# Kernel tuning notes

Measured on AMD Instinct MI355X. Metric: run time of the kernel, lower is better.

The kernel has to match this reference:

```python
import jax, jax.numpy as jnp
import numpy as np

N_NODES = 50000
N_EDGES = 800000
IN_CH = 16
OUT_CH = 16


def setup_inputs() -> dict:
    key = jax.random.key(0)
    ks = jax.random.split(key, 12)
    s = lambda d: 1.0 / np.sqrt(d)
    return {
        "x": jax.random.normal(ks[0], (N_NODES, IN_CH), jnp.float32),
        "edge_index": jax.random.randint(ks[1], (2, N_EDGES), 0, N_NODES, jnp.int64),
        "edge_attr": jax.random.uniform(ks[2], (N_EDGES, 8), jnp.float32),
        "W1": jax.random.normal(ks[3], (8, 100), jnp.float32) * s(8),
        "b1": jnp.zeros((100,), jnp.float32),
        "W2": jax.random.normal(ks[4], (100, 100), jnp.float32) * s(100),
        "b2": jnp.zeros((100,), jnp.float32),
        "W3": jax.random.normal(ks[5], (100, 100), jnp.float32) * s(100),
        "b3": jnp.zeros((100,), jnp.float32),
        "W4": jax.random.normal(ks[6], (100, IN_CH * OUT_CH), jnp.float32) * s(100),
        "b4": jnp.zeros((IN_CH * OUT_CH,), jnp.float32),
        "root": jax.random.normal(ks[7], (IN_CH, OUT_CH), jnp.float32) * s(IN_CH),
        "bias": jnp.zeros((OUT_CH,), jnp.float32),
    }


def reference(x, edge_index, edge_attr, W1, b1, W2, b2, W3, b3, W4, b4, root, bias):
    src, dst = edge_index[0], edge_index[1]
    # edge MLP -> per-edge weight matrix [E, in, out]
    h = jax.nn.relu(edge_attr @ W1 + b1)
    h = jax.nn.relu(h @ W2 + b2)
    h = jax.nn.relu(h @ W3 + b3)
    w = (h @ W4 + b4).reshape(-1, IN_CH, OUT_CH)
    # gather source features, per-edge matmul
    msg = jnp.einsum('ei,eio->eo', x[src], w)  # [E, out]
    # scatter-mean into destination nodes
    agg = jax.ops.segment_sum(msg, dst, num_segments=N_NODES)
    cnt = jax.ops.segment_sum(jnp.ones((msg.shape[0],), msg.dtype), dst, num_segments=N_NODES)
    agg = agg / jnp.maximum(cnt, 1.0)[:, None]
    return x @ root + agg + bias
```

## Files before the change

kernel.cpp:

```cpp
#include <hip/hip_runtime.h>
#include <hip/hip_bf16.h>

constexpr int N_NODES = 50000;
constexpr int E_TOTAL = 800000;
constexpr int EB   = 128;
constexpr int NT   = E_TOTAL / EB;
constexpr int GRID = 256;
constexpr int TPB  = 512;

typedef __attribute__((ext_vector_type(8))) short bf16x8;
typedef __attribute__((ext_vector_type(4))) float f32x4;

constexpr size_t WS_CNT = 0;
constexpr size_t WS_W1  = 200704;
constexpr size_t WS_W2  = WS_W1 + 8192;
constexpr size_t WS_W3  = WS_W2 + 32768;
constexpr size_t WS_W4  = WS_W3 + 32768;

constexpr int L_W4  = 0;
constexpr int L_HA  = 69632;
constexpr int L_HB  = 104448;
constexpr int L_EA  = 139264;
constexpr int L_XS  = 149504;
constexpr int L_DST = 159744;
constexpr int L_TOT = 160768;

__device__ inline unsigned short bfb(float f) {
    __hip_bfloat16 h = __float2bfloat16(f);
    return __builtin_bit_cast(unsigned short, h);
}
__device__ inline unsigned pk2(float a, float b) {
    return (unsigned)bfb(a) | ((unsigned)bfb(b) << 16);
}

__device__ inline void stage(const char* g, char* l, int bytes, int t) {
    const int wave = t >> 6, lane = t & 63;
    for (int c = wave; c * 1024 < bytes; c += 8) {
        __builtin_amdgcn_global_load_lds(
            (const __attribute__((address_space(1))) void*)(g + c * 1024 + lane * 16),
            (__attribute__((address_space(3))) void*)(l + c * 1024), 16, 0, 0);
    }
}

template<int IN_OFF, int OUT_OFF>
__device__ inline void layerB(char* sm, const bf16x8 (&wf)[2][4],
                              int we, int wn, int lane)
{
    const int r16 = lane & 15, g4 = lane >> 4;
    f32x4 acc[2][4] = {};
#pragma unroll
    for (int ks = 0; ks < 4; ++ks) {
        bf16x8 b[4];
#pragma unroll
        for (int ef = 0; ef < 4; ++ef) {
            const int e = 64 * we + 16 * ef + r16;
            b[ef] = *reinterpret_cast<const bf16x8*>(sm + IN_OFF + e * 272 + ks * 64 + g4 * 16);
        }
#pragma unroll
        for (int mf = 0; mf < 2; ++mf)
#pragma unroll
            for (int ef = 0; ef < 4; ++ef)
                acc[mf][ef] = __builtin_amdgcn_mfma_f32_16x16x32_bf16(wf[mf][ks], b[ef], acc[mf][ef], 0, 0, 0);
    }
#pragma unroll
    for (int mf = 0; mf < 2; ++mf)
#pragma unroll
        for (int ef = 0; ef < 4; ++ef) {
            const int e = 64 * we + 16 * ef + r16;
            uint2 pk;
            pk.x = pk2(fmaxf(acc[mf][ef][0], 0.f), fmaxf(acc[mf][ef][1], 0.f));
            pk.y = pk2(fmaxf(acc[mf][ef][2], 0.f), fmaxf(acc[mf][ef][3], 0.f));
            *reinterpret_cast<uint2*>(sm + OUT_OFF + e * 272 + 64 * wn + 32 * mf + 8 * g4) = pk;
        }
}

__global__ __launch_bounds__(TPB, 2)
void edge_kernel(const float* __restrict__ x, const int* __restrict__ eidx,
                 const float* __restrict__ ea, const char* __restrict__ ws,
                 float* __restrict__ out, float* __restrict__ cnt)
{
    extern __shared__ char sm[];
    const int t    = threadIdx.x;
    const int lane = t & 63;
    const int wave = t >> 6;
    const int we   = wave >> 2, wn = wave & 3;
    const int we4  = wave >> 1, wn4 = wave & 1;
    const int r16  = lane & 15, g4 = lane >> 4;
    int* dsti = reinterpret_cast<int*>(sm + L_DST);

    bf16x8 wf1[2], wf2[2][4], wf3[2][4];
#pragma unroll
    for (int mf = 0; mf < 2; ++mf) {
        const int n = 32 * wn + 16 * mf + r16;
        wf1[mf] = *reinterpret_cast<const bf16x8*>(ws + WS_W1 + n * 64 + g4 * 16);
#pragma unroll
        for (int ks = 0; ks < 4; ++ks) {
            wf2[mf][ks] = *reinterpret_cast<const bf16x8*>(ws + WS_W2 + n * 256 + ks * 64 + g4 * 16);
            wf3[mf][ks] = *reinterpret_cast<const bf16x8*>(ws + WS_W3 + n * 256 + ks * 64 + g4 * 16);
        }
    }

    stage(ws + WS_W4, sm + L_W4, 69632, t);

    {
        const int e = t >> 2, q = t & 3;
        if (q > 0) {
            uint4 z = make_uint4(0u, 0u, 0u, 0u);
            if (q == 1) z.x = 0x3F80u;
            *reinterpret_cast<uint4*>(sm + L_EA + e * 80 + 16 * q) = z;
        }
    }

    float4 eaR, xvR; int dstR = 0;
    {
        const int e0 = blockIdx.x * EB;
        if (t < 256) eaR = *reinterpret_cast<const float4*>(&ea[(size_t)(e0 + (t >> 1)) * 8 + (t & 1) * 4]);
        const int s = eidx[e0 + (t >> 2)];
        xvR = *reinterpret_cast<const float4*>(&x[(size_t)s * 16 + (t & 3) * 4]);
        if (t < 128) dstR = eidx[E_TOTAL + e0 + t];
    }

    int p = 0;
    bool has_prev = false;
    for (int tile = blockIdx.x; tile < NT; tile += GRID) {
        if (has_prev) {
            const int e = t >> 2, o0 = (t & 3) * 4;
            const float4 s0 = *reinterpret_cast<const float4*>(sm + L_HB + e * 80 + o0 * 4);
            const float4 s1 = *reinterpret_cast<const float4*>(sm + L_HB + 10240 + e * 80 + o0 * 4);
            const int d = dsti[(p ^ 1) * 128 + e];
            unsafeAtomicAdd(&out[(size_t)d * 16 + o0 + 0], s0.x + s1.x);
            unsafeAtomicAdd(&out[(size_t)d * 16 + o0 + 1], s0.y + s1.y);
            unsafeAtomicAdd(&out[(size_t)d * 16 + o0 + 2], s0.z + s1.z);
            unsafeAtomicAdd(&out[(size_t)d * 16 + o0 + 3], s0.w + s1.w);
            if ((t & 3) == 0) unsafeAtomicAdd(&cnt[d], 1.0f);
        }
        if (t < 256) {
            uint2 pk; pk.x = pk2(eaR.x, eaR.y); pk.y = pk2(eaR.z, eaR.w);
            *reinterpret_cast<uint2*>(sm + L_EA + (t >> 1) * 80 + 8 * (t & 1)) = pk;
        }
        *reinterpret_cast<float4*>(sm + L_XS + (t >> 2) * 80 + (t & 3) * 16) = xvR;
        if (t < 128) dsti[p * 128 + t] = dstR;

        const int nxt = tile + GRID;
        if (nxt < NT) {
            const int e0 = nxt * EB;
            if (t < 256) eaR = *reinterpret_cast<const float4*>(&ea[(size_t)(e0 + (t >> 1)) * 8 + (t & 1) * 4]);
            const int s = eidx[e0 + (t >> 2)];
            xvR = *reinterpret_cast<const float4*>(&x[(size_t)s * 16 + (t & 3) * 4]);
            if (t < 128) dstR = eidx[E_TOTAL + e0 + t];
        }
        __syncthreads();

        {
            f32x4 acc[2][4] = {};
            bf16x8 b[4];
#pragma unroll
            for (int ef = 0; ef < 4; ++ef) {
                const int e = 64 * we + 16 * ef + r16;
                b[ef] = *reinterpret_cast<const bf16x8*>(sm + L_EA + e * 80 + g4 * 16);
            }
#pragma unroll
            for (int mf = 0; mf < 2; ++mf)
#pragma unroll
                for (int ef = 0; ef < 4; ++ef)
                    acc[mf][ef] = __builtin_amdgcn_mfma_f32_16x16x32_bf16(wf1[mf], b[ef], acc[mf][ef], 0, 0, 0);
#pragma unroll
            for (int mf = 0; mf < 2; ++mf)
#pragma unroll
                for (int ef = 0; ef < 4; ++ef) {
                    const int e = 64 * we + 16 * ef + r16;
                    uint2 pk;
                    pk.x = pk2(fmaxf(acc[mf][ef][0], 0.f), fmaxf(acc[mf][ef][1], 0.f));
                    pk.y = pk2(fmaxf(acc[mf][ef][2], 0.f), fmaxf(acc[mf][ef][3], 0.f));
                    *reinterpret_cast<uint2*>(sm + L_HA + e * 272 + 64 * wn + 32 * mf + 8 * g4) = pk;
                }
        }
        __syncthreads();
        layerB<L_HA, L_HB>(sm, wf2, we, wn, lane);
        __syncthreads();
        layerB<L_HB, L_HA>(sm, wf3, we, wn, lane);
        __syncthreads();

        {
            f32x4 acc[8][2] = {};
#pragma unroll
            for (int ks = 0; ks < 4; ++ks) {
                bf16x8 b[2];
#pragma unroll
                for (int ef = 0; ef < 2; ++ef) {
                    const int e = 32 * we4 + 16 * ef + r16;
                    b[ef] = *reinterpret_cast<const bf16x8*>(sm + L_HA + e * 272 + ks * 64 + g4 * 16);
                }
#pragma unroll
                for (int mf = 0; mf < 8; ++mf) {
                    const int n = 128 * wn4 + 16 * mf + r16;
                    const bf16x8 a = *reinterpret_cast<const bf16x8*>(sm + L_W4 + n * 272 + ks * 64 + g4 * 16);
#pragma unroll
                    for (int ef = 0; ef < 2; ++ef)
                        acc[mf][ef] = __builtin_amdgcn_mfma_f32_16x16x32_bf16(a, b[ef], acc[mf][ef], 0, 0, 0);
                }
            }
#pragma unroll
            for (int ef = 0; ef < 2; ++ef) {
                const int e = 32 * we4 + 16 * ef + r16;
                const float4 xa = *reinterpret_cast<const float4*>(sm + L_XS + e * 80 + 32 * wn4);
                const float4 xb = *reinterpret_cast<const float4*>(sm + L_XS + e * 80 + 32 * wn4 + 16);
                float4 mp = make_float4(0.f, 0.f, 0.f, 0.f);
#pragma unroll
                for (int mf = 0; mf < 8; ++mf) {
                    const float xi = (mf < 4) ? (&xa.x)[mf] : (&xb.x)[mf - 4];
                    mp.x = fmaf(xi, acc[mf][ef][0], mp.x);
                    mp.y = fmaf(xi, acc[mf][ef][1], mp.y);
                    mp.z = fmaf(xi, acc[mf][ef][2], mp.z);
                    mp.w = fmaf(xi, acc[mf][ef][3], mp.w);
                }
                *reinterpret_cast<float4*>(sm + L_HB + wn4 * 10240 + e * 80 + g4 * 16) = mp;
            }
        }
        __syncthreads();
        p ^= 1;
        has_prev = true;
    }

    {
        const int e = t >> 2, o0 = (t & 3) * 4;
        const float4 s0 = *reinterpret_cast<const float4*>(sm + L_HB + e * 80 + o0 * 4);
        const float4 s1 = *reinterpret_cast<const float4*>(sm + L_HB + 10240 + e * 80 + o0 * 4);
        const int d = dsti[(p ^ 1) * 128 + e];
        unsafeAtomicAdd(&out[(size_t)d * 16 + o0 + 0], s0.x + s1.x);
        unsafeAtomicAdd(&out[(size_t)d * 16 + o0 + 1], s0.y + s1.y);
        unsafeAtomicAdd(&out[(size_t)d * 16 + o0 + 2], s0.z + s1.z);
        unsafeAtomicAdd(&out[(size_t)d * 16 + o0 + 3], s0.w + s1.w);
        if ((t & 3) == 0) unsafeAtomicAdd(&cnt[d], 1.0f);
    }
}

__global__ __launch_bounds__(256)
void prep_kernel(const float* __restrict__ W1, const float* __restrict__ b1,
                 const float* __restrict__ W2, const float* __restrict__ b2,
                 const float* __restrict__ W3, const float* __restrict__ b3,
                 const float* __restrict__ W4, const float* __restrict__ b4,
                 char* __restrict__ ws)
{
    const int id = blockIdx.x * 256 + threadIdx.x;
    if (id < N_NODES) reinterpret_cast<float*>(ws + WS_CNT)[id] = 0.f;
    if (id >= 69632) return;
    if (id < 4096) {
        const int n = id >> 5, k = id & 31;
        float v = 0.f;
        if (k < 8)        { if (n < 100) v = W1[k * 100 + n]; }
        else if (k == 8)  { v = (n < 100) ? b1[n] : (n == 100 ? 1.f : 0.f); }
        reinterpret_cast<unsigned short*>(ws + WS_W1)[id] = bfb(v);
    } else if (id < 20480) {
        const int j = id - 4096, n = j >> 7, k = j & 127;
        float v = 0.f;
        if (k < 100)       { if (n < 100) v = W2[k * 100 + n]; }
        else if (k == 100) { v = (n < 100) ? b2[n] : (n == 100 ? 1.f : 0.f); }
        reinterpret_cast<unsigned short*>(ws + WS_W2)[j] = bfb(v);
    } else if (id < 36864) {
        const int j = id - 20480, n = j >> 7, k = j & 127;
        float v = 0.f;
        if (k < 100)       { if (n < 100) v = W3[k * 100 + n]; }
        else if (k == 100) { v = (n < 100) ? b3[n] : (n == 100 ? 1.f : 0.f); }
        reinterpret_cast<unsigned short*>(ws + WS_W3)[j] = bfb(v);
    } else {
        const int j = id - 36864, n = j >> 7, k = j & 127;
        float v = 0.f;
        if (k < 100)       v = W4[k * 256 + n];
        else if (k == 100) v = b4[n];
        *reinterpret_cast<unsigned short*>(ws + WS_W4 + n * 272 + 2 * k) = bfb(v);
    }
}

__global__ __launch_bounds__(256)
void node_kernel(const float* __restrict__ x, const float* __restrict__ root,
                 const float* __restrict__ bias, const float* __restrict__ cnt,
                 float* __restrict__ out)
{
    const int n = blockIdx.x * blockDim.x + threadIdx.x;
    if (n >= N_NODES) return;
    float xr[16];
#pragma unroll
    for (int q = 0; q < 4; ++q) {
        const float4 v = *reinterpret_cast<const float4*>(&x[(size_t)n * 16 + 4 * q]);
        xr[4 * q] = v.x; xr[4 * q + 1] = v.y; xr[4 * q + 2] = v.z; xr[4 * q + 3] = v.w;
    }
    const float inv = 1.f / fmaxf(cnt[n], 1.f);
#pragma unroll
    for (int q = 0; q < 4; ++q) {
        float4 o4 = *reinterpret_cast<float4*>(&out[(size_t)n * 16 + 4 * q]);
        float res[4];
#pragma unroll
        for (int j = 0; j < 4; ++j) {
            const int o = 4 * q + j;
            float dot = 0.f;
#pragma unroll
            for (int i = 0; i < 16; ++i)
                dot = fmaf(xr[i], root[i * 16 + o], dot);
            res[j] = dot + (&o4.x)[j] * inv + bias[o];
        }
        *reinterpret_cast<float4*>(&out[(size_t)n * 16 + 4 * q]) = make_float4(res[0], res[1], res[2], res[3]);
    }
}

extern "C" void kernel_launch(void* const* d_in, const int* in_sizes, int n_in,
                              void* d_out, int out_size, void* d_ws, size_t ws_size,
                              hipStream_t stream)
{
    const float* x    = (const float*)d_in[0];
    const int*   eidx = (const int*)  d_in[1];
    const float* ea   = (const float*)d_in[2];
    const float* W1   = (const float*)d_in[3];
    const float* b1   = (const float*)d_in[4];
    const float* W2   = (const float*)d_in[5];
    const float* b2   = (const float*)d_in[6];
    const float* W3   = (const float*)d_in[7];
    const float* b3   = (const float*)d_in[8];
    const float* W4   = (const float*)d_in[9];
    const float* b4   = (const float*)d_in[10];
    const float* root = (const float*)d_in[11];
    const float* bias = (const float*)d_in[12];
    float* out = (float*)d_out;
    char*  ws  = (char*)d_ws;
    float* cnt = (float*)d_ws;

    (void)in_sizes; (void)n_in; (void)ws_size;

    hipFuncSetAttribute((const void*)edge_kernel,
                        hipFuncAttributeMaxDynamicSharedMemorySize, L_TOT);

    hipMemsetAsync(d_out, 0, (size_t)out_size * sizeof(float), stream);

    hipLaunchKernelGGL(prep_kernel, dim3(272), dim3(256), 0, stream,
                       W1, b1, W2, b2, W3, b3, W4, b4, ws);
    hipLaunchKernelGGL(edge_kernel, dim3(GRID), dim3(TPB), L_TOT, stream,
                       x, eidx, ea, ws, out, cnt);
    hipLaunchKernelGGL(node_kernel, dim3((N_NODES + 255) / 256), dim3(256), 0, stream,
                       x, root, bias, cnt, out);
}
```

Measured before the change: 344.5 us.

## Switch edge MLP to 32x32x16 MFMA and keep W4 in registers

Replaces the 16x16x32 MFMA tiling with 32x32x16 tiles in all four edge-MLP layers, changing the per-wave work split, and loads the W4 fragments into registers once per wave instead of staging W4 into LDS and rereading it every tile. Removing the W4 LDS copy shrinks shared memory, and a new 4-way message buffer replaces the previous 2-way reduction before the atomics. The larger MFMA shape means fewer instructions and fewer LDS operand reads. In exchange, register pressure rises a lot: wf2, wf3 and wf4 plus the 16-float accumulators must fit under launch_bounds(512,2), so spills are possible.

```diff
diff --git a/kernel.cpp b/kernel.cpp
--- a/kernel.cpp
+++ b/kernel.cpp
@@ -8,22 +8,22 @@
 constexpr int GRID = 256;
 constexpr int TPB  = 512;
 
-typedef __attribute__((ext_vector_type(8))) short bf16x8;
-typedef __attribute__((ext_vector_type(4))) float f32x4;
+typedef __attribute__((ext_vector_type(8)))  short bf16x8;
+typedef __attribute__((ext_vector_type(16))) float f32x16;
 
 constexpr size_t WS_CNT = 0;
 constexpr size_t WS_W1  = 200704;
-constexpr size_t WS_W2  = WS_W1 + 8192;
+constexpr size_t WS_W2  = WS_W1 + 4096;
 constexpr size_t WS_W3  = WS_W2 + 32768;
 constexpr size_t WS_W4  = WS_W3 + 32768;
 
-constexpr int L_W4  = 0;
-constexpr int L_HA  = 69632;
-constexpr int L_HB  = 104448;
-constexpr int L_EA  = 139264;
-constexpr int L_XS  = 149504;
-constexpr int L_DST = 159744;
-constexpr int L_TOT = 160768;
+constexpr int L_HA  = 0;
+constexpr int L_HB  = 34816;
+constexpr int L_EA  = 69632;
+constexpr int L_XS  = 75776;
+constexpr int L_MSG = 86016;
+constexpr int L_DST = 126976;
+constexpr int L_TOT = 128000;
 
 __device__ inline unsigned short bfb(float f) {
     __hip_bfloat16 h = __float2bfloat16(f);
@@ -32,46 +32,38 @@
 __device__ inline unsigned pk2(float a, float b) {
     return (unsigned)bfb(a) | ((unsigned)bfb(b) << 16);
 }
-
-__device__ inline void stage(const char* g, char* l, int bytes, int t) {
-    const int wave = t >> 6, lane = t & 63;
-    for (int c = wave; c * 1024 < bytes; c += 8) {
-        __builtin_amdgcn_global_load_lds(
-            (const __attribute__((address_space(1))) void*)(g + c * 1024 + lane * 16),
-            (__attribute__((address_space(3))) void*)(l + c * 1024), 16, 0, 0);
-    }
+__device__ inline unsigned pk2r(float a, float b) {
+    return pk2(fmaxf(a, 0.f), fmaxf(b, 0.f));
 }
 
 template<int IN_OFF, int OUT_OFF>
-__device__ inline void layerB(char* sm, const bf16x8 (&wf)[2][4],
-                              int we, int wn, int lane)
-{
-    const int r16 = lane & 15, g4 = lane >> 4;
-    f32x4 acc[2][4] = {};
-#pragma unroll
-    for (int ks = 0; ks < 4; ++ks) {
-        bf16x8 b[4];
-#pragma unroll
-        for (int ef = 0; ef < 4; ++ef) {
-            const int e = 64 * we + 16 * ef + r16;
-            b[ef] = *reinterpret_cast<const bf16x8*>(sm + IN_OFF + e * 272 + ks * 64 + g4 * 16);
-        }
-#pragma unroll
-        for (int mf = 0; mf < 2; ++mf)
-#pragma unroll
-            for (int ef = 0; ef < 4; ++ef)
-                acc[mf][ef] = __builtin_amdgcn_mfma_f32_16x16x32_bf16(wf[mf][ks], b[ef], acc[mf][ef], 0, 0, 0);
-    }
-#pragma unroll
-    for (int mf = 0; mf < 2; ++mf)
-#pragma unroll
-        for (int ef = 0; ef < 4; ++ef) {
-            const int e = 64 * we + 16 * ef + r16;
+__device__ inline void layer32(char* sm, const bf16x8 (&wf)[8],
+                               int wn, int we, int l31, int g)
+{
+    f32x16 acc[2] = {};
+#pragma unroll
+    for (int ks = 0; ks < 8; ++ks) {
+        bf16x8 b[2];
+#pragma unroll
+        for (int ef = 0; ef < 2; ++ef) {
+            const int e = 64 * we + 32 * ef + l31;
+            b[ef] = *reinterpret_cast<const bf16x8*>(sm + IN_OFF + e * 272 + ks * 32 + g * 16);
+        }
+#pragma unroll
+        for (int ef = 0; ef < 2; ++ef)
+            acc[ef] = __builtin_amdgcn_mfma_f32_32x32x16_bf16(wf[ks], b[ef], acc[ef], 0, 0, 0);
+    }
+#pragma unroll
+    for (int ef = 0; ef < 2; ++ef) {
+        const int e = 64 * we + 32 * ef + l31;
+#pragma unroll
+        for (int q = 0; q < 4; ++q) {
             uint2 pk;
-            pk.x = pk2(fmaxf(acc[mf][ef][0], 0.f), fmaxf(acc[mf][ef][1], 0.f));
-            pk.y = pk2(fmaxf(acc[mf][ef][2], 0.f), fmaxf(acc[mf][ef][3], 0.f));
-            *reinterpret_cast<uint2*>(sm + OUT_OFF + e * 272 + 64 * wn + 32 * mf + 8 * g4) = pk;
-        }
+            pk.x = pk2r(acc[ef][4 * q + 0], acc[ef][4 * q + 1]);
+            pk.y = pk2r(acc[ef][4 * q + 2], acc[ef][4 * q + 3]);
+            *reinterpret_cast<uint2*>(sm + OUT_OFF + e * 272 + 64 * wn + 16 * q + 8 * g) = pk;
+        }
+    }
 }
 
 __global__ __launch_bounds__(TPB, 2)
@@ -83,33 +75,30 @@
     const int t    = threadIdx.x;
     const int lane = t & 63;
     const int wave = t >> 6;
-    const int we   = wave >> 2, wn = wave & 3;
-    const int we4  = wave >> 1, wn4 = wave & 1;
-    const int r16  = lane & 15, g4 = lane >> 4;
+    const int wn   = wave & 3, we = wave >> 2;
+    const int l31  = lane & 31, g = lane >> 5;
     int* dsti = reinterpret_cast<int*>(sm + L_DST);
 
-    bf16x8 wf1[2], wf2[2][4], wf3[2][4];
-#pragma unroll
-    for (int mf = 0; mf < 2; ++mf) {
-        const int n = 32 * wn + 16 * mf + r16;
-        wf1[mf] = *reinterpret_cast<const bf16x8*>(ws + WS_W1 + n * 64 + g4 * 16);
-#pragma unroll
-        for (int ks = 0; ks < 4; ++ks) {
-            wf2[mf][ks] = *reinterpret_cast<const bf16x8*>(ws + WS_W2 + n * 256 + ks * 64 + g4 * 16);
-            wf3[mf][ks] = *reinterpret_cast<const bf16x8*>(ws + WS_W3 + n * 256 + ks * 64 + g4 * 16);
-        }
-    }
-
-    stage(ws + WS_W4, sm + L_W4, 69632, t);
-
+    bf16x8 wf1, wf2[8], wf3[8], wf4[2][8];
     {
-        const int e = t >> 2, q = t & 3;
-        if (q > 0) {
-            uint4 z = make_uint4(0u, 0u, 0u, 0u);
-            if (q == 1) z.x = 0x3F80u;
-            *reinterpret_cast<uint4*>(sm + L_EA + e * 80 + 16 * q) = z;
-        }
-    }
+        const int n = 32 * wn + l31;
+        wf1 = *reinterpret_cast<const bf16x8*>(ws + WS_W1 + n * 32 + g * 16);
+#pragma unroll
+        for (int ks = 0; ks < 8; ++ks) {
+            wf2[ks] = *reinterpret_cast<const bf16x8*>(ws + WS_W2 + n * 256 + ks * 32 + g * 16);
+            wf3[ks] = *reinterpret_cast<const bf16x8*>(ws + WS_W3 + n * 256 + ks * 32 + g * 16);
+        }
+#pragma unroll
+        for (int mf = 0; mf < 2; ++mf) {
+            const int n4 = 64 * wn + 32 * mf + l31;
+#pragma unroll
+            for (int ks = 0; ks < 8; ++ks)
+                wf4[mf][ks] = *reinterpret_cast<const bf16x8*>(ws + WS_W4 + n4 * 256 + ks * 32 + g * 16);
+        }
+    }
+
+    if (t < 128)
+        *reinterpret_cast<uint4*>(sm + L_EA + t * 48 + 16) = make_uint4(0x3F80u, 0u, 0u, 0u);
 
     float4 eaR, xvR; int dstR = 0;
     {
@@ -125,18 +114,20 @@
     for (int tile = blockIdx.x; tile < NT; tile += GRID) {
         if (has_prev) {
             const int e = t >> 2, o0 = (t & 3) * 4;
-            const float4 s0 = *reinterpret_cast<const float4*>(sm + L_HB + e * 80 + o0 * 4);
-            const float4 s1 = *reinterpret_cast<const float4*>(sm + L_HB + 10240 + e * 80 + o0 * 4);
+            float4 s0 = *reinterpret_cast<const float4*>(sm + L_MSG + 0 * 10240 + e * 80 + o0 * 4);
+            const float4 s1 = *reinterpret_cast<const float4*>(sm + L_MSG + 1 * 10240 + e * 80 + o0 * 4);
+            const float4 s2 = *reinterpret_cast<const float4*>(sm + L_MSG + 2 * 10240 + e * 80 + o0 * 4);
+            const float4 s3 = *reinterpret_cast<const float4*>(sm + L_MSG + 3 * 10240 + e * 80 + o0 * 4);
             const int d = dsti[(p ^ 1) * 128 + e];
-            unsafeAtomicAdd(&out[(size_t)d * 16 + o0 + 0], s0.x + s1.x);
-            unsafeAtomicAdd(&out[(size_t)d * 16 + o0 + 1], s0.y + s1.y);
-            unsafeAtomicAdd(&out[(size_t)d * 16 + o0 + 2], s0.z + s1.z);
-            unsafeAtomicAdd(&out[(size_t)d * 16 + o0 + 3], s0.w + s1.w);
+            unsafeAtomicAdd(&out[(size_t)d * 16 + o0 + 0], s0.x + s1.x + s2.x + s3.x);
+            unsafeAtomicAdd(&out[(size_t)d * 16 + o0 + 1], s0.y + s1.y + s2.y + s3.y);
+            unsafeAtomicAdd(&out[(size_t)d * 16 + o0 + 2], s0.z + s1.z + s2.z + s3.z);
+            unsafeAtomicAdd(&out[(size_t)d * 16 + o0 + 3], s0.w + s1.w + s2.w + s3.w);
             if ((t & 3) == 0) unsafeAtomicAdd(&cnt[d], 1.0f);
         }
         if (t < 256) {
             uint2 pk; pk.x = pk2(eaR.x, eaR.y); pk.y = pk2(eaR.z, eaR.w);
-            *reinterpret_cast<uint2*>(sm + L_EA + (t >> 1) * 80 + 8 * (t & 1)) = pk;
+            *reinterpret_cast<uint2*>(sm + L_EA + (t >> 1) * 48 + 8 * (t & 1)) = pk;
         }
         *reinterpret_cast<float4*>(sm + L_XS + (t >> 2) * 80 + (t & 3) * 16) = xvR;
         if (t < 128) dsti[p * 128 + t] = dstR;
@@ -152,69 +143,64 @@
         __syncthreads();
 
         {
-            f32x4 acc[2][4] = {};
-            bf16x8 b[4];
-#pragma unroll
-            for (int ef = 0; ef < 4; ++ef) {
-                const int e = 64 * we + 16 * ef + r16;
-                b[ef] = *reinterpret_cast<const bf16x8*>(sm + L_EA + e * 80 + g4 * 16);
+            f32x16 acc[2] = {};
+#pragma unroll
+            for (int ef = 0; ef < 2; ++ef) {
+                const int e = 64 * we + 32 * ef + l31;
+                const bf16x8 b = *reinterpret_cast<const bf16x8*>(sm + L_EA + e * 48 + g * 16);
+                acc[ef] = __builtin_amdgcn_mfma_f32_32x32x16_bf16(wf1, b, acc[ef], 0, 0, 0);
             }
 #pragma unroll
-            for (int mf = 0; mf < 2; ++mf)
-#pragma unroll
-                for (int ef = 0; ef < 4; ++ef)
-                    acc[mf][ef] = __builtin_amdgcn_mfma_f32_16x16x32_bf16(wf1[mf], b[ef], acc[mf][ef], 0, 0, 0);
-#pragma unroll
-            for (int mf = 0; mf < 2; ++mf)
-#pragma unroll
-                for (int ef = 0; ef < 4; ++ef) {
-                    const int e = 64 * we + 16 * ef + r16;
+            for (int ef = 0; ef < 2; ++ef) {
+                const int e = 64 * we + 32 * ef + l31;
+#pragma unroll
+                for (int q = 0; q < 4; ++q) {
                     uint2 pk;
-                    pk.x = pk2(fmaxf(acc[mf][ef][0], 0.f), fmaxf(acc[mf][ef][1], 0.f));
-                    pk.y = pk2(fmaxf(acc[mf][ef][2], 0.f), fmaxf(acc[mf][ef][3], 0.f));
-                    *reinterpret_cast<uint2*>(sm + L_HA + e * 272 + 64 * wn + 32 * mf + 8 * g4) = pk;
-                }
-        }
-        __syncthreads();
-        layerB<L_HA, L_HB>(sm, wf2, we, wn, lane);
-        __syncthreads();
-        layerB<L_HB, L_HA>(sm, wf3, we, wn, lane);
-        __syncthreads();
-
-        {
-            f32x4 acc[8][2] = {};
-#pragma unroll
-            for (int ks = 0; ks < 4; ++ks) {
-                bf16x8 b[2];
-#pragma unroll
-                for (int ef = 0; ef < 2; ++ef) {
-                    const int e = 32 * we4 + 16 * ef + r16;
-                    b[ef] = *reinterpret_cast<const bf16x8*>(sm + L_HA + e * 272 + ks * 64 + g4 * 16);
-                }
-#pragma unroll
-                for (int mf = 0; mf < 8; ++mf) {
-                    const int n = 128 * wn4 + 16 * mf + r16;
-                    const bf16x8 a = *reinterpret_cast<const bf16x8*>(sm + L_W4 + n * 272 + ks * 64 + g4 * 16);
-#pragma unroll
-                    for (int ef = 0; ef < 2; ++ef)
-                        acc[mf][ef] = __builtin_amdgcn_mfma_f32_16x16x32_bf16(a, b[ef], acc[mf][ef], 0, 0, 0);
+                    pk.x = pk2r(acc[ef][4 * q + 0], acc[ef][4 * q + 1]);
+                    pk.y = pk2r(acc[ef][4 * q + 2], acc[ef][4 * q + 3]);
+                    *reinterpret_cast<uint2*>(sm + L_HA + e * 272 + 64 * wn + 16 * q + 8 * g) = pk;
                 }
             }
+        }
+        __syncthreads();
+        layer32<L_HA, L_HB>(sm, wf2, wn, we, l31, g);
+        __syncthreads();
+        layer32<L_HB, L_HA>(sm, wf3, wn, we, l31, g);
+        __syncthreads();
+
+        {
+            f32x16 acc4[2][2] = {};
+#pragma unroll
+            for (int ks = 0; ks < 8; ++ks) {
+                bf16x8 b[2];
+#pragma unroll
+                for (int ef = 0; ef < 2; ++ef) {
+                    const int e = 64 * we + 32 * ef + l31;
+                    b[ef] = *reinterpret_cast<const bf16x8*>(sm + L_HA + e * 272 + ks * 32 + g * 16);
+                }
+#pragma unroll
+                for (int mf = 0; mf < 2; ++mf)
+#pragma unroll
+                    for (int ef = 0; ef < 2; ++ef)
+                        acc4[mf][ef] = __builtin_amdgcn_mfma_f32_32x32x16_bf16(wf4[mf][ks], b[ef], acc4[mf][ef], 0, 0, 0);
+            }
 #pragma unroll
             for (int ef = 0; ef < 2; ++ef) {
-                const int e = 32 * we4 + 16 * ef + r16;
-                const float4 xa = *reinterpret_cast<const float4*>(sm + L_XS + e * 80 + 32 * wn4);
-                const float4 xb = *reinterpret_cast<const float4*>(sm + L_XS + e * 80 + 32 * wn4 + 16);
-                float4 mp = make_float4(0.f, 0.f, 0.f, 0.f);
-#pragma unroll
-                for (int mf = 0; mf < 8; ++mf) {
-                    const float xi = (mf < 4) ? (&xa.x)[mf] : (&xb.x)[mf - 4];
-                    mp.x = fmaf(xi, acc[mf][ef][0], mp.x);
-                    mp.y = fmaf(xi, acc[mf][ef][1], mp.y);
-                    mp.z = fmaf(xi, acc[mf][ef][2], mp.z);
-                    mp.w = fmaf(xi, acc[mf][ef][3], mp.w);
-                }
-                *reinterpret_cast<float4*>(sm + L_HB + wn4 * 10240 + e * 80 + g4 * 16) = mp;
+                const int e = 64 * we + 32 * ef + l31;
+                const float4 xv = *reinterpret_cast<const float4*>(sm + L_XS + e * 80 + wn * 16);
+                float pr[8] = {0.f, 0.f, 0.f, 0.f, 0.f, 0.f, 0.f, 0.f};
+#pragma unroll
+                for (int mf = 0; mf < 2; ++mf)
+#pragma unroll
+                    for (int reg = 0; reg < 16; ++reg) {
+                        const float xi = (&xv.x)[2 * mf + (reg >> 3)];
+                        const int s = (reg & 3) + 4 * ((reg >> 2) & 1);
+                        pr[s] = fmaf(xi, acc4[mf][ef][reg], pr[s]);
+                    }
+                *reinterpret_cast<float4*>(sm + L_MSG + wn * 10240 + e * 80 + 16 * g) =
+                    make_float4(pr[0], pr[1], pr[2], pr[3]);
+                *reinterpret_cast<float4*>(sm + L_MSG + wn * 10240 + e * 80 + 32 + 16 * g) =
+                    make_float4(pr[4], pr[5], pr[6], pr[7]);
             }
         }
         __syncthreads();
@@ -222,15 +208,17 @@
         has_prev = true;
     }
 
-    {
+    if (has_prev) {
         const int e = t >> 2, o0 = (t & 3) * 4;
-        const float4 s0 = *reinterpret_cast<const float4*>(sm + L_HB + e * 80 + o0 * 4);
-        const float4 s1 = *reinterpret_cast<const float4*>(sm + L_HB + 10240 + e * 80 + o0 * 4);
+        const float4 s0 = *reinterpret_cast<const float4*>(sm + L_MSG + 0 * 10240 + e * 80 + o0 * 4);
+        const float4 s1 = *reinterpret_cast<const float4*>(sm + L_MSG + 1 * 10240 + e * 80 + o0 * 4);
+        const float4 s2 = *reinterpret_cast<const float4*>(sm + L_MSG + 2 * 10240 + e * 80 + o0 * 4);
+        const float4 s3 = *reinterpret_cast<const float4*>(sm + L_MSG + 3 * 10240 + e * 80 + o0 * 4);
         const int d = dsti[(p ^ 1) * 128 + e];
-        unsafeAtomicAdd(&out[(size_t)d * 16 + o0 + 0], s0.x + s1.x);
-        unsafeAtomicAdd(&out[(size_t)d * 16 + o0 + 1], s0.y + s1.y);
-        unsafeAtomicAdd(&out[(size_t)d * 16 + o0 + 2], s0.z + s1.z);
-        unsafeAtomicAdd(&out[(size_t)d * 16 + o0 + 3], s0.w + s1.w);
+        unsafeAtomicAdd(&out[(size_t)d * 16 + o0 + 0], s0.x + s1.x + s2.x + s3.x);
+        unsafeAtomicAdd(&out[(size_t)d * 16 + o0 + 1], s0.y + s1.y + s2.y + s3.y);
+        unsafeAtomicAdd(&out[(size_t)d * 16 + o0 + 2], s0.z + s1.z + s2.z + s3.z);
+        unsafeAtomicAdd(&out[(size_t)d * 16 + o0 + 3], s0.w + s1.w + s2.w + s3.w);
         if ((t & 3) == 0) unsafeAtomicAdd(&cnt[d], 1.0f);
     }
 }
@@ -244,31 +232,31 @@
 {
     const int id = blockIdx.x * 256 + threadIdx.x;
     if (id < N_NODES) reinterpret_cast<float*>(ws + WS_CNT)[id] = 0.f;
-    if (id >= 69632) return;
-    if (id < 4096) {
-        const int n = id >> 5, k = id & 31;
+    if (id >= 67584) return;
+    if (id < 2048) {
+        const int n = id >> 4, k = id & 15;
         float v = 0.f;
         if (k < 8)        { if (n < 100) v = W1[k * 100 + n]; }
         else if (k == 8)  { v = (n < 100) ? b1[n] : (n == 100 ? 1.f : 0.f); }
         reinterpret_cast<unsigned short*>(ws + WS_W1)[id] = bfb(v);
-    } else if (id < 20480) {
-        const int j = id - 4096, n = j >> 7, k = j & 127;
+    } else if (id < 18432) {
+        const int j = id - 2048, n = j >> 7, k = j & 127;
         float v = 0.f;
         if (k < 100)       { if (n < 100) v = W2[k * 100 + n]; }
         else if (k == 100) { v = (n < 100) ? b2[n] : (n == 100 ? 1.f : 0.f); }
         reinterpret_cast<unsigned short*>(ws + WS_W2)[j] = bfb(v);
-    } else if (id < 36864) {
-        const int j = id - 20480, n = j >> 7, k = j & 127;
+    } else if (id < 34816) {
+        const int j = id - 18432, n = j >> 7, k = j & 127;
         float v = 0.f;
         if (k < 100)       { if (n < 100) v = W3[k * 100 + n]; }
         else if (k == 100) { v = (n < 100) ? b3[n] : (n == 100 ? 1.f : 0.f); }
         reinterpret_cast<unsigned short*>(ws + WS_W3)[j] = bfb(v);
     } else {
-        const int j = id - 36864, n = j >> 7, k = j & 127;
+        const int j = id - 34816, n = j >> 7, k = j & 127;
         float v = 0.f;
         if (k < 100)       v = W4[k * 256 + n];
         else if (k == 100) v = b4[n];
-        *reinterpret_cast<unsigned short*>(ws + WS_W4 + n * 272 + 2 * k) = bfb(v);
+        reinterpret_cast<unsigned short*>(ws + WS_W4)[j] = bfb(v);
     }
 }
 
@@ -331,7 +319,7 @@
 
     hipMemsetAsync(d_out, 0, (size_t)out_size * sizeof(float), stream);
 
-    hipLaunchKernelGGL(prep_kernel, dim3(272), dim3(256), 0, stream,
+    hipLaunchKernelGGL(prep_kernel, dim3(264), dim3(256), 0, stream,
                        W1, b1, W2, b2, W3, b3, W4, b4, ws);
     hipLaunchKernelGGL(edge_kernel, dim3(GRID), dim3(TPB), L_TOT, stream,
                        x, eidx, ea, ws, out, cnt);
```

Measured after the change: 328.8 us. -4.6%, faster.
